# Performance work log

Measured on AMD Instinct MI355X. Metric: run time of the kernel, lower is better.

The kernel has to match this reference:

```python
import jax, jax.numpy as jnp
import numpy as np

B, S, H, E = 64, 512, 768, 8
HID = 256

def setup_inputs() -> dict:
    key = jax.random.key(0)
    ks = jax.random.split(key, 20)
    seq = jax.random.normal(ks[0], (B, S, H), dtype=jnp.float32)
    starts = jax.random.randint(ks[1], (B, E), 0, S - 16)
    spans = jax.random.randint(ks[2], (B, E), 0, 12)
    ends = jnp.minimum(starts + spans, S - 1)
    w = lambda k, shp: (jax.random.normal(k, shp, dtype=jnp.float32) * 0.02)
    return {
        "sequence_output": seq,
        "entity_start_positions": starts,
        "entity_end_positions": ends,
        "mW1": w(ks[3], (3 * H, HID)), "mb1": jnp.zeros((HID,), jnp.float32),
        "mW2": w(ks[4], (HID, 3)),     "mb2": jnp.zeros((3,), jnp.float32),
        "pW1": w(ks[5], (3 * H, HID)), "pb1": jnp.zeros((HID,), jnp.float32),
        "pW2": w(ks[6], (HID, 6)),     "pb2": jnp.zeros((6,), jnp.float32),
        "aW1": w(ks[7], (3 * H, HID)), "ab1": jnp.zeros((HID,), jnp.float32),
        "aW2": w(ks[8], (HID, 12)),    "ab2": jnp.zeros((12,), jnp.float32),
        "iW1": w(ks[9], (3 * H, HID)), "ib1": jnp.zeros((HID,), jnp.float32),
        "iW2": w(ks[10], (HID, 4)),    "ib2": jnp.zeros((4,), jnp.float32),
    }

def _mlp(x, W1, b1, W2, b2):
    return jax.nn.relu(x @ W1 + b1) @ W2 + b2  # dropout is inference no-op

def reference(sequence_output, entity_start_positions, entity_end_positions,
              mW1, mb1, mW2, mb2, pW1, pb1, pW2, pb2,
              aW1, ab1, aW2, ab2, iW1, ib1, iW2, ib2):
    Bs, Ss, Hs = sequence_output.shape
    dt = sequence_output.dtype
    # prefix sums: P[b, t] = sum of tokens [0, t)
    P = jnp.concatenate([jnp.zeros((Bs, 1, Hs), dt), jnp.cumsum(sequence_output, axis=1)], axis=1)  # [B,S+1,H]
    s = entity_start_positions  # [B,E]
    e = entity_end_positions    # [B,E]
    bidx = jnp.arange(Bs)[:, None]
    Ps = P[bidx, s]          # [B,E,H] sum of tokens [0, start)
    Pe1 = P[bidx, e + 1]     # [B,E,H] sum of tokens [0, end+1)
    Ptot = P[:, Ss][:, None, :]  # [B,1,H]
    left_n = s.astype(dt)[..., None]
    span_n = (e - s + 1).astype(dt)[..., None]
    right_cnt = (Ss - (e + 1))
    right_n = right_cnt.astype(dt)[..., None]
    left = jnp.where(s[..., None] > 0, Ps / jnp.maximum(left_n, 1.0), 0.0)
    span = (Pe1 - Ps) / span_n
    right = jnp.where(right_cnt[..., None] > 0, (Ptot - Pe1) / jnp.maximum(right_n, 1.0), 0.0)
    emb = jnp.concatenate([left, span, right], axis=-1).reshape(-1, 3 * Hs)  # [N, 3H]
    main_logits = _mlp(emb, mW1, mb1, mW2, mb2)            # [N,3]
    main_probs = jax.nn.softmax(main_logits, axis=-1)
    pred = jnp.argmax(main_probs, axis=-1)                 # [N]
    lp = jax.nn.sigmoid(_mlp(emb, pW1, pb1, pW2, pb2))     # [N,6]
    la = jax.nn.sigmoid(_mlp(emb, aW1, ab1, aW2, ab2))     # [N,12]
    li = jax.nn.sigmoid(_mlp(emb, iW1, ib1, iW2, ib2))     # [N,4]
    fp = jnp.pad(lp, ((0, 0), (0, 16)))
    fa = jnp.pad(la, ((0, 0), (6, 4)))
    fi = jnp.pad(li, ((0, 0), (18, 0)))
    r = pred[:, None]
    fine = jnp.where(r == 0, fp, jnp.where(r == 1, fa, fi))  # [N,22]
    return main_logits, main_probs, fine
```

## Files before the change

### kernel.cpp

```cpp
#include <hip/hip_runtime.h>

#define HH   768
#define SS   512
#define BB   64
#define NE   512
#define K3   2304
#define HID  256
#define NCH  16
#define CRW  32
#define NCOL 1280

typedef __attribute__((ext_vector_type(4))) float  f32x4;
typedef _Float16 f16;
typedef __attribute__((ext_vector_type(8))) _Float16 f16x8;
typedef __attribute__((ext_vector_type(4))) _Float16 f16x4;

__global__ __launch_bounds__(192) void k_scan(
    const float* __restrict__ seq, const int* __restrict__ starts,
    const int* __restrict__ ends, const float* __restrict__ pW1,
    const float* __restrict__ aW1, const float* __restrict__ iW1,
    const float* __restrict__ mW1,
    float* __restrict__ chunkSum, float* __restrict__ cap,
    f16* __restrict__ wT)
{
  __shared__ float Ls[48 * 65];
  const int bx = blockIdx.x;
  const int t  = threadIdx.x;

  if (bx < BB * NCH) {
    const int b = bx >> 4, c = bx & 15;
    int ev[16];
#pragma unroll
    for (int j = 0; j < 8; j++) {
      ev[j]     = starts[b * 8 + j];
      ev[8 + j] = ends[b * 8 + j] + 1;
    }
    unsigned rowhit = 0;
#pragma unroll
    for (int j = 0; j < 16; j++) {
      const int d = ev[j] - c * CRW;
      if ((unsigned)d < 32u) rowhit |= (1u << d);
    }
    const float* base = seq + ((size_t)(b * SS + c * CRW)) * HH + t * 4;
    f32x4 run = {0.f, 0.f, 0.f, 0.f};
#pragma unroll 8
    for (int r = 0; r < CRW; r++) {
      const int s = c * CRW + r;
      if (rowhit & (1u << r)) {
#pragma unroll
        for (int j = 0; j < 16; j++) {
          if (ev[j] == s)
            *(f32x4*)(cap + ((size_t)(b * 16 + j)) * HH + t * 4) = run;
        }
      }
      f32x4 v = *(const f32x4*)(base + (size_t)r * HH);
      run += v;
    }
    *(f32x4*)(chunkSum + ((size_t)(b * 16 + c)) * HH + t * 4) = run;
  } else {
    const int bi   = bx - BB * NCH;
    const int slot = bi / 192;
    const int r    = bi % 192;
    const int kt = r >> 2, nt = r & 3;
    const int k0 = kt * 48, n0 = nt * 64;
    const float* W = (slot == 0) ? pW1 : ((slot == 1) ? aW1 :
                     ((slot == 2) ? iW1 : mW1));
#pragma unroll
    for (int p = 0; p < 4; p++) {
      const int row = (t >> 4) + p * 12;
      const int col = (t & 15) * 4;
      f32x4 v = *(const f32x4*)(W + (size_t)(k0 + row) * HID + n0 + col);
      Ls[row * 65 + col + 0] = v.x;
      Ls[row * 65 + col + 1] = v.y;
      Ls[row * 65 + col + 2] = v.z;
      Ls[row * 65 + col + 3] = v.w;
    }
    __syncthreads();
    const int n = t / 3, u = t % 3;
#pragma unroll
    for (int j = 0; j < 2; j++) {
      const int kb = u * 16 + j * 8;
      f16x8 pk;
#pragma unroll
      for (int i = 0; i < 8; i++) {
        float x = Ls[(kb + i) * 65 + n];
        if (slot == 4) { const f16 h = (f16)x; x = x - (float)h; }
        pk[i] = (f16)x;
      }
      *(f16x8*)(wT + (size_t)(slot * 256 + n0 + n) * K3 + k0 + kb) = pk;
    }
  }
}

__global__ __launch_bounds__(192) void k_emb(
    const float* __restrict__ chunkSum, const float* __restrict__ cap,
    const int* __restrict__ starts, const int* __restrict__ ends,
    f16* __restrict__ embH)
{
  const int bx = blockIdx.x;
  const int t  = threadIdx.x;
  const int b = bx >> 3, e = bx & 7;
  const int s  = starts[b * 8 + e];
  const int en = ends[b * 8 + e];
  const int cs = s >> 5, ce = (en + 1) >> 5;

  const float* csb = chunkSum + (size_t)(b * 16) * HH + t * 4;
  f32x4 acc = {0.f, 0.f, 0.f, 0.f};
  f32x4 baseS = {0.f, 0.f, 0.f, 0.f}, baseE = {0.f, 0.f, 0.f, 0.f};
#pragma unroll
  for (int c = 0; c < 16; c++) {
    if (c == cs) baseS = acc;
    if (c == ce) baseE = acc;
    acc += *(const f32x4*)(csb + (size_t)c * HH);
  }
  f32x4 capS = *(const f32x4*)(cap + (size_t)(b * 16 + e) * HH + t * 4);
  f32x4 capE = *(const f32x4*)(cap + (size_t)(b * 16 + 8 + e) * HH + t * 4);
  f32x4 Ps = baseS + capS;
  f32x4 Pe = baseE + capE;
  f32x4 Pt = acc;

  f32x4 zero = {0.f, 0.f, 0.f, 0.f};
  f32x4 left = zero;
  if (s > 0) left = Ps * (1.0f / (float)s);
  f32x4 span = (Pe - Ps) * (1.0f / (float)(en - s + 1));
  const int rc = SS - (en + 1);
  f32x4 right = zero;
  if (rc > 0) right = (Pt - Pe) * (1.0f / (float)rc);

  f16* ob = embH + (size_t)bx * K3 + t * 4;
  f16x4 p0, p1, p2;
#pragma unroll
  for (int i = 0; i < 4; i++) {
    p0[i] = (f16)left[i];
    p1[i] = (f16)span[i];
    p2[i] = (f16)right[i];
  }
  *(f16x4*)(ob)        = p0;
  *(f16x4*)(ob + 768)  = p1;
  *(f16x4*)(ob + 1536) = p2;
}

__global__ __launch_bounds__(256) void k_gemm(
    const f16* __restrict__ embH, const f16* __restrict__ wT,
    float* __restrict__ Hall)
{
  __shared__ __align__(16) char smem[27648];
  const int bx0 = blockIdx.x;
  const int bx  = (bx0 & 7) * 40 + (bx0 >> 3);
  const int t  = threadIdx.x;
  const int mt = bx & 15, nt = bx >> 4;
  const int m0 = mt * 32, nG0 = nt * 64;

  const int l = t & 63, w = t >> 6;
  const int w2 = w & 1;
  const int kw = w >> 1;
  const int klane = l >> 4;
  const int lr = l & 15;
  f32x4 acc[2][2] = {};

  const int am = t >> 3, ako = (t & 7) * 8;
  const f16* gA = embH + (size_t)(m0 + am) * K3 + ako;
  const int aoff = am * 72 + ako;
  const int bn0 = t >> 3,        bko0 = (t & 7) * 8;
  const int bn1 = (t + 256) >> 3, bko1 = (t & 7) * 8;
  const f16* gB0 = wT + (size_t)(nG0 + bn0) * K3 + bko0;
  const f16* gB1 = wT + (size_t)(nG0 + bn1) * K3 + bko1;
  const int boff0 = bn0 * 72 + bko0, boff1 = bn1 * 72 + bko1;

  f16x8 pA, pB0, pB1, qA, qB0, qB1;

#define LOADSET(S, KT) { const int kn_ = (KT) * 64;                       \
    S##A  = *(const f16x8*)(gA  + kn_);                                   \
    S##B0 = *(const f16x8*)(gB0 + kn_);                                   \
    S##B1 = *(const f16x8*)(gB1 + kn_); }

#define WRITESET(S, BUF) { f16* An_ = (f16*)(smem + (BUF) * 13824);       \
    f16* Bn_ = An_ + 2304;                                                \
    *(f16x8*)(An_ + aoff)  = S##A;                                        \
    *(f16x8*)(Bn_ + boff0) = S##B0;                                       \
    *(f16x8*)(Bn_ + boff1) = S##B1; }

#define COMPUTE(BUF) { f16* Ac_ = (f16*)(smem + (BUF) * 13824);           \
    f16* Bc_ = Ac_ + 2304;                                                \
    const int koff_ = kw * 32 + klane * 8;                                \
    f16x8 aW[2], bE[2];                                                   \
    _Pragma("unroll")                                                     \
    for (int f = 0; f < 2; f++) {                                         \
      aW[f] = *(const f16x8*)(Bc_ + (w2 * 32 + f * 16 + lr) * 72 + koff_);\
      bE[f] = *(const f16x8*)(Ac_ + (f * 16 + lr) * 72 + koff_);          \
    }                                                                     \
    _Pragma("unroll")                                                     \
    for (int fn = 0; fn < 2; fn++)                                        \
      _Pragma("unroll")                                                   \
      for (int fm = 0; fm < 2; fm++)                                      \
        acc[fn][fm] = __builtin_amdgcn_mfma_f32_16x16x32_f16(             \
            aW[fn], bE[fm], acc[fn][fm], 0, 0, 0); }

  LOADSET(p, 0);
  LOADSET(q, 1);
  WRITESET(p, 0);
  __syncthreads();

  for (int kt = 0; kt < 36; kt += 2) {
    if (kt < 34) LOADSET(p, kt + 2);
    COMPUTE(0);
    WRITESET(q, 1);
    __syncthreads();
    if (kt < 34) LOADSET(q, kt + 3);
    COMPUTE(1);
    if (kt < 34) WRITESET(p, 0);
    __syncthreads();
  }
#undef LOADSET
#undef WRITESET
#undef COMPUTE

  float* Lt = (float*)smem;
  if (kw == 1) {
#pragma unroll
    for (int fn = 0; fn < 2; fn++)
#pragma unroll
      for (int fm = 0; fm < 2; fm++) {
        const int nl = w2 * 32 + fn * 16 + klane * 4;
        const int ml = fm * 16 + lr;
        *(f32x4*)(Lt + ml * 68 + nl) = acc[fn][fm];
      }
  }
  __syncthreads();
  if (kw == 0) {
#pragma unroll
    for (int fn = 0; fn < 2; fn++)
#pragma unroll
      for (int fm = 0; fm < 2; fm++) {
        const int nl = w2 * 32 + fn * 16 + klane * 4;
        const int ml = fm * 16 + lr;
        f32x4* pd = (f32x4*)(Lt + ml * 68 + nl);
        *pd = *pd + acc[fn][fm];
      }
  }
  __syncthreads();
  const int row = t >> 3, cb = (t & 7) * 8;
  float* dst = Hall + (size_t)(m0 + row) * NCOL + nG0 + cb;
  const float* src = Lt + row * 68 + cb;
  *(f32x4*)(dst)     = *(const f32x4*)(src);
  *(f32x4*)(dst + 4) = *(const f32x4*)(src + 4);
}

__global__ __launch_bounds__(256) void k_head(
    const float* __restrict__ Hall,
    const float* __restrict__ mb1, const float* __restrict__ mW2, const float* __restrict__ mb2,
    const float* __restrict__ pb1, const float* __restrict__ pW2, const float* __restrict__ pb2,
    const float* __restrict__ ab1, const float* __restrict__ aW2, const float* __restrict__ ab2,
    const float* __restrict__ ib1, const float* __restrict__ iW2, const float* __restrict__ ib2,
    float* __restrict__ out)
{
  __shared__ float red[4][15];
  const int m = blockIdx.x;
  const int t = threadIdx.x;
  const int l = t & 63, wi = t >> 6;
  const int n = t;
  const float* hrow = Hall + (size_t)m * NCOL;

  float h = hrow[768 + n] + hrow[1024 + n] + mb1[n];
  h = h > 0.f ? h : 0.f;
  float am0 = h * mW2[n * 3 + 0];
  float am1 = h * mW2[n * 3 + 1];
  float am2 = h * mW2[n * 3 + 2];

  float hp = hrow[n] + pb1[n];
  hp = hp > 0.f ? hp : 0.f;
  float ha = hrow[256 + n] + ab1[n];
  ha = ha > 0.f ? ha : 0.f;
  float hv = hrow[512 + n] + ib1[n];
  hv = hv > 0.f ? hv : 0.f;

#pragma unroll
  for (int d = 1; d < 64; d <<= 1) {
    am0 += __shfl_xor(am0, d);
    am1 += __shfl_xor(am1, d);
    am2 += __shfl_xor(am2, d);
  }
  if (l == 0) { red[wi][0] = am0; red[wi][1] = am1; red[wi][2] = am2; }
  __syncthreads();

  const float l0 = red[0][0] + red[1][0] + red[2][0] + red[3][0] + mb2[0];
  const float l1 = red[0][1] + red[1][1] + red[2][1] + red[3][1] + mb2[1];
  const float l2 = red[0][2] + red[1][2] + red[2][2] + red[3][2] + mb2[2];
  int pred = 0;
  {
    float pbv = l0;
    if (l1 > pbv) { pbv = l1; pred = 1; }
    if (l2 > pbv) { pbv = l2; pred = 2; }
  }

  if (pred == 0) {
    float ap[6];
#pragma unroll
    for (int o = 0; o < 6; o++) ap[o] = hp * pW2[n * 6 + o];
#pragma unroll
    for (int d = 1; d < 64; d <<= 1)
#pragma unroll
      for (int o = 0; o < 6; o++) ap[o] += __shfl_xor(ap[o], d);
    if (l == 0)
#pragma unroll
      for (int o = 0; o < 6; o++) red[wi][3 + o] = ap[o];
  } else if (pred == 1) {
    float aa[12];
#pragma unroll
    for (int o = 0; o < 12; o++) aa[o] = ha * aW2[n * 12 + o];
#pragma unroll
    for (int d = 1; d < 64; d <<= 1)
#pragma unroll
      for (int o = 0; o < 12; o++) aa[o] += __shfl_xor(aa[o], d);
    if (l == 0)
#pragma unroll
      for (int o = 0; o < 12; o++) red[wi][3 + o] = aa[o];
  } else {
    float ai[4];
#pragma unroll
    for (int o = 0; o < 4; o++) ai[o] = hv * iW2[n * 4 + o];
#pragma unroll
    for (int d = 1; d < 64; d <<= 1)
#pragma unroll
      for (int o = 0; o < 4; o++) ai[o] += __shfl_xor(ai[o], d);
    if (l == 0)
#pragma unroll
      for (int o = 0; o < 4; o++) red[wi][3 + o] = ai[o];
  }
  __syncthreads();

  if (t == 0) {
    const float mx = fmaxf(l0, fmaxf(l1, l2));
    const float e0 = expf(l0 - mx), e1 = expf(l1 - mx), e2 = expf(l2 - mx);
    const float inv = 1.0f / (e0 + e1 + e2);
    const float p0 = e0 * inv, p1 = e1 * inv, p2 = e2 * inv;

    out[m * 3 + 0] = l0;
    out[m * 3 + 1] = l1;
    out[m * 3 + 2] = l2;
    out[1536 + m * 3 + 0] = p0;
    out[1536 + m * 3 + 1] = p1;
    out[1536 + m * 3 + 2] = p2;

    float f[22];
#pragma unroll
    for (int j = 0; j < 22; j++) f[j] = 0.f;
    if (pred == 0) {
#pragma unroll
      for (int j = 0; j < 6; j++) {
        const float v = red[0][3 + j] + red[1][3 + j] + red[2][3 + j] + red[3][3 + j];
        f[j] = 1.0f / (1.0f + expf(-(v + pb2[j])));
      }
    } else if (pred == 1) {
#pragma unroll
      for (int j = 0; j < 12; j++) {
        const float v = red[0][3 + j] + red[1][3 + j] + red[2][3 + j] + red[3][3 + j];
        f[6 + j] = 1.0f / (1.0f + expf(-(v + ab2[j])));
      }
    } else {
#pragma unroll
      for (int j = 0; j < 4; j++) {
        const float v = red[0][3 + j] + red[1][3 + j] + red[2][3 + j] + red[3][3 + j];
        f[18 + j] = 1.0f / (1.0f + expf(-(v + ib2[j])));
      }
    }
#pragma unroll
    for (int j = 0; j < 22; j++) out[3072 + m * 22 + j] = f[j];
  }
}

extern "C" void kernel_launch(void* const* d_in, const int* in_sizes, int n_in,
                              void* d_out, int out_size, void* d_ws, size_t ws_size,
                              hipStream_t stream)
{
  const float* seq    = (const float*)d_in[0];
  const int*   starts = (const int*)d_in[1];
  const int*   ends   = (const int*)d_in[2];
  const float* mW1 = (const float*)d_in[3];
  const float* mb1 = (const float*)d_in[4];
  const float* mW2 = (const float*)d_in[5];
  const float* mb2 = (const float*)d_in[6];
  const float* pW1 = (const float*)d_in[7];
  const float* pb1 = (const float*)d_in[8];
  const float* pW2 = (const float*)d_in[9];
  const float* pb2 = (const float*)d_in[10];
  const float* aW1 = (const float*)d_in[11];
  const float* ab1 = (const float*)d_in[12];
  const float* aW2 = (const float*)d_in[13];
  const float* ab2 = (const float*)d_in[14];
  const float* iW1 = (const float*)d_in[15];
  const float* ib1 = (const float*)d_in[16];
  const float* iW2 = (const float*)d_in[17];
  const float* ib2 = (const float*)d_in[18];

  char* ws = (char*)d_ws;
  float* chunkSum = (float*)(ws);
  float* cap      = (float*)(ws + 3145728);
  f16*   embH     = (f16*)(ws + 6291456);
  f16*   wT       = (f16*)(ws + 8650752);
  float* Hall     = (float*)(ws + 14548992);

  k_scan<<<dim3(1984), dim3(192), 0, stream>>>(seq, starts, ends, pW1, aW1, iW1, mW1,
                                               chunkSum, cap, wT);
  k_emb<<<dim3(512), dim3(192), 0, stream>>>(chunkSum, cap, starts, ends, embH);
  k_gemm<<<dim3(320), dim3(256), 0, stream>>>(embH, wT, Hall);
  k_head<<<dim3(512), dim3(256), 0, stream>>>(Hall,
                                              mb1, mW2, mb2, pb1, pW2, pb2,
                                              ab1, aW2, ab2, ib1, iW2, ib2,
                                              (float*)d_out);
}
```

Before: 49.61 us.

## Split GEMM K dimension in two, merge emb blocks per batch, fuse hi/lo weight split

The GEMM now splits the K=2304 reduction into two halves across twice as many blocks (640). Each half writes its own partial Hall buffer, and the head kernel sums the two. The emb kernel goes from one block per entity to one block per batch: it stages the 16 chunk sums in shared memory and loops over 8 entities, so the chunk sums are read once per batch instead of once per entity. The scan kernel writes the fp16 high and low parts of mW1 from a single block, cutting the weight-transpose grid. The costs are extra Hall write traffic and a much smaller emb grid, only 64 blocks.

```diff
diff --git a/kernel.cpp b/kernel.cpp
--- a/kernel.cpp
+++ b/kernel.cpp
@@ -77,17 +77,30 @@
     }
     __syncthreads();
     const int n = t / 3, u = t % 3;
-#pragma unroll
-    for (int j = 0; j < 2; j++) {
-      const int kb = u * 16 + j * 8;
-      f16x8 pk;
-#pragma unroll
-      for (int i = 0; i < 8; i++) {
-        float x = Ls[(kb + i) * 65 + n];
-        if (slot == 4) { const f16 h = (f16)x; x = x - (float)h; }
-        pk[i] = (f16)x;
-      }
-      *(f16x8*)(wT + (size_t)(slot * 256 + n0 + n) * K3 + k0 + kb) = pk;
+    if (slot < 3) {
+#pragma unroll
+      for (int j = 0; j < 2; j++) {
+        const int kb = u * 16 + j * 8;
+        f16x8 pk;
+#pragma unroll
+        for (int i = 0; i < 8; i++) pk[i] = (f16)Ls[(kb + i) * 65 + n];
+        *(f16x8*)(wT + (size_t)(slot * 256 + n0 + n) * K3 + k0 + kb) = pk;
+      }
+    } else {
+#pragma unroll
+      for (int j = 0; j < 2; j++) {
+        const int kb = u * 16 + j * 8;
+        f16x8 ph, pl;
+#pragma unroll
+        for (int i = 0; i < 8; i++) {
+          const float x = Ls[(kb + i) * 65 + n];
+          const f16 h = (f16)x;
+          ph[i] = h;
+          pl[i] = (f16)(x - (float)h);
+        }
+        *(f16x8*)(wT + (size_t)(768  + n0 + n) * K3 + k0 + kb) = ph;
+        *(f16x8*)(wT + (size_t)(1024 + n0 + n) * K3 + k0 + kb) = pl;
+      }
     }
   }
 }
@@ -97,47 +110,55 @@
     const int* __restrict__ starts, const int* __restrict__ ends,
     f16* __restrict__ embH)
 {
-  const int bx = blockIdx.x;
-  const int t  = threadIdx.x;
-  const int b = bx >> 3, e = bx & 7;
-  const int s  = starts[b * 8 + e];
-  const int en = ends[b * 8 + e];
-  const int cs = s >> 5, ce = (en + 1) >> 5;
-
-  const float* csb = chunkSum + (size_t)(b * 16) * HH + t * 4;
-  f32x4 acc = {0.f, 0.f, 0.f, 0.f};
-  f32x4 baseS = {0.f, 0.f, 0.f, 0.f}, baseE = {0.f, 0.f, 0.f, 0.f};
-#pragma unroll
-  for (int c = 0; c < 16; c++) {
-    if (c == cs) baseS = acc;
-    if (c == ce) baseE = acc;
-    acc += *(const f32x4*)(csb + (size_t)c * HH);
-  }
-  f32x4 capS = *(const f32x4*)(cap + (size_t)(b * 16 + e) * HH + t * 4);
-  f32x4 capE = *(const f32x4*)(cap + (size_t)(b * 16 + 8 + e) * HH + t * 4);
-  f32x4 Ps = baseS + capS;
-  f32x4 Pe = baseE + capE;
-  f32x4 Pt = acc;
-
-  f32x4 zero = {0.f, 0.f, 0.f, 0.f};
-  f32x4 left = zero;
-  if (s > 0) left = Ps * (1.0f / (float)s);
-  f32x4 span = (Pe - Ps) * (1.0f / (float)(en - s + 1));
-  const int rc = SS - (en + 1);
-  f32x4 right = zero;
-  if (rc > 0) right = (Pt - Pe) * (1.0f / (float)rc);
-
-  f16* ob = embH + (size_t)bx * K3 + t * 4;
-  f16x4 p0, p1, p2;
-#pragma unroll
-  for (int i = 0; i < 4; i++) {
-    p0[i] = (f16)left[i];
-    p1[i] = (f16)span[i];
-    p2[i] = (f16)right[i];
-  }
-  *(f16x4*)(ob)        = p0;
-  *(f16x4*)(ob + 768)  = p1;
-  *(f16x4*)(ob + 1536) = p2;
+  __shared__ float Ls[16 * 768];
+  const int b = blockIdx.x;
+  const int t = threadIdx.x;
+
+#pragma unroll
+  for (int c = 0; c < 16; c++)
+    *(f32x4*)(Ls + c * 768 + t * 4) =
+        *(const f32x4*)(chunkSum + ((size_t)(b * 16 + c)) * HH + t * 4);
+  __syncthreads();
+
+  for (int e = 0; e < 8; e++) {
+    const int s  = starts[b * 8 + e];
+    const int en = ends[b * 8 + e];
+    const int cs = s >> 5, ce = (en + 1) >> 5;
+
+    f32x4 acc = {0.f, 0.f, 0.f, 0.f};
+    f32x4 baseS = {0.f, 0.f, 0.f, 0.f}, baseE = {0.f, 0.f, 0.f, 0.f};
+#pragma unroll
+    for (int c = 0; c < 16; c++) {
+      if (c == cs) baseS = acc;
+      if (c == ce) baseE = acc;
+      acc += *(const f32x4*)(Ls + c * 768 + t * 4);
+    }
+    f32x4 capS = *(const f32x4*)(cap + (size_t)(b * 16 + e) * HH + t * 4);
+    f32x4 capE = *(const f32x4*)(cap + (size_t)(b * 16 + 8 + e) * HH + t * 4);
+    f32x4 Ps = baseS + capS;
+    f32x4 Pe = baseE + capE;
+    f32x4 Pt = acc;
+
+    f32x4 zero = {0.f, 0.f, 0.f, 0.f};
+    f32x4 left = zero;
+    if (s > 0) left = Ps * (1.0f / (float)s);
+    f32x4 span = (Pe - Ps) * (1.0f / (float)(en - s + 1));
+    const int rc = SS - (en + 1);
+    f32x4 right = zero;
+    if (rc > 0) right = (Pt - Pe) * (1.0f / (float)rc);
+
+    f16* ob = embH + (size_t)(b * 8 + e) * K3 + t * 4;
+    f16x4 p0, p1, p2;
+#pragma unroll
+    for (int i = 0; i < 4; i++) {
+      p0[i] = (f16)left[i];
+      p1[i] = (f16)span[i];
+      p2[i] = (f16)right[i];
+    }
+    *(f16x4*)(ob)        = p0;
+    *(f16x4*)(ob + 768)  = p1;
+    *(f16x4*)(ob + 1536) = p2;
+  }
 }
 
 __global__ __launch_bounds__(256) void k_gemm(
@@ -146,10 +167,13 @@
 {
   __shared__ __align__(16) char smem[27648];
   const int bx0 = blockIdx.x;
-  const int bx  = (bx0 & 7) * 40 + (bx0 >> 3);
+  const int bx  = (bx0 & 7) * 80 + (bx0 >> 3);
   const int t  = threadIdx.x;
-  const int mt = bx & 15, nt = bx >> 4;
+  const int mt = bx & 15;
+  const int rest = bx >> 4;
+  const int ks = rest / 20, nt = rest % 20;
   const int m0 = mt * 32, nG0 = nt * 64;
+  const int kc0 = ks * 1152;
 
   const int l = t & 63, w = t >> 6;
   const int w2 = w & 1;
@@ -159,12 +183,12 @@
   f32x4 acc[2][2] = {};
 
   const int am = t >> 3, ako = (t & 7) * 8;
-  const f16* gA = embH + (size_t)(m0 + am) * K3 + ako;
+  const f16* gA = embH + (size_t)(m0 + am) * K3 + kc0 + ako;
   const int aoff = am * 72 + ako;
-  const int bn0 = t >> 3,        bko0 = (t & 7) * 8;
+  const int bn0 = t >> 3,         bko0 = (t & 7) * 8;
   const int bn1 = (t + 256) >> 3, bko1 = (t & 7) * 8;
-  const f16* gB0 = wT + (size_t)(nG0 + bn0) * K3 + bko0;
-  const f16* gB1 = wT + (size_t)(nG0 + bn1) * K3 + bko1;
+  const f16* gB0 = wT + (size_t)(nG0 + bn0) * K3 + kc0 + bko0;
+  const f16* gB1 = wT + (size_t)(nG0 + bn1) * K3 + kc0 + bko1;
   const int boff0 = bn0 * 72 + bko0, boff1 = bn1 * 72 + bko1;
 
   f16x8 pA, pB0, pB1, qA, qB0, qB1;
@@ -201,14 +225,14 @@
   WRITESET(p, 0);
   __syncthreads();
 
-  for (int kt = 0; kt < 36; kt += 2) {
-    if (kt < 34) LOADSET(p, kt + 2);
+  for (int kt = 0; kt < 18; kt += 2) {
+    if (kt < 16) LOADSET(p, kt + 2);
     COMPUTE(0);
     WRITESET(q, 1);
     __syncthreads();
-    if (kt < 34) LOADSET(q, kt + 3);
+    if (kt < 16) LOADSET(q, kt + 3);
     COMPUTE(1);
-    if (kt < 34) WRITESET(p, 0);
+    if (kt < 16) WRITESET(p, 0);
     __syncthreads();
   }
 #undef LOADSET
@@ -240,7 +264,7 @@
   }
   __syncthreads();
   const int row = t >> 3, cb = (t & 7) * 8;
-  float* dst = Hall + (size_t)(m0 + row) * NCOL + nG0 + cb;
+  float* dst = Hall + (size_t)ks * NE * NCOL + (size_t)(m0 + row) * NCOL + nG0 + cb;
   const float* src = Lt + row * 68 + cb;
   *(f32x4*)(dst)     = *(const f32x4*)(src);
   *(f32x4*)(dst + 4) = *(const f32x4*)(src + 4);
@@ -259,19 +283,20 @@
   const int t = threadIdx.x;
   const int l = t & 63, wi = t >> 6;
   const int n = t;
-  const float* hrow = Hall + (size_t)m * NCOL;
-
-  float h = hrow[768 + n] + hrow[1024 + n] + mb1[n];
+  const float* hrA = Hall + (size_t)m * NCOL;
+  const float* hrB = Hall + (size_t)NE * NCOL + (size_t)m * NCOL;
+
+  float h = (hrA[768 + n] + hrB[768 + n]) + (hrA[1024 + n] + hrB[1024 + n]) + mb1[n];
   h = h > 0.f ? h : 0.f;
   float am0 = h * mW2[n * 3 + 0];
   float am1 = h * mW2[n * 3 + 1];
   float am2 = h * mW2[n * 3 + 2];
 
-  float hp = hrow[n] + pb1[n];
+  float hp = (hrA[n] + hrB[n]) + pb1[n];
   hp = hp > 0.f ? hp : 0.f;
-  float ha = hrow[256 + n] + ab1[n];
+  float ha = (hrA[256 + n] + hrB[256 + n]) + ab1[n];
   ha = ha > 0.f ? ha : 0.f;
-  float hv = hrow[512 + n] + ib1[n];
+  float hv = (hrA[512 + n] + hrB[512 + n]) + ib1[n];
   hv = hv > 0.f ? hv : 0.f;
 
 #pragma unroll
@@ -400,10 +425,10 @@
   f16*   wT       = (f16*)(ws + 8650752);
   float* Hall     = (float*)(ws + 14548992);
 
-  k_scan<<<dim3(1984), dim3(192), 0, stream>>>(seq, starts, ends, pW1, aW1, iW1, mW1,
+  k_scan<<<dim3(1792), dim3(192), 0, stream>>>(seq, starts, ends, pW1, aW1, iW1, mW1,
                                                chunkSum, cap, wT);
-  k_emb<<<dim3(512), dim3(192), 0, stream>>>(chunkSum, cap, starts, ends, embH);
-  k_gemm<<<dim3(320), dim3(256), 0, stream>>>(embH, wT, Hall);
+  k_emb<<<dim3(64), dim3(192), 0, stream>>>(chunkSum, cap, starts, ends, embH);
+  k_gemm<<<dim3(640), dim3(256), 0, stream>>>(embH, wT, Hall);
   k_head<<<dim3(512), dim3(256), 0, stream>>>(Hall,
                                               mb1, mW2, mb2, pb1, pW2, pb2,
                                               ab1, aW2, ab2, ib1, iW2, ib2,
```

Measured after the change: 51.78 us. +4.4%, slower.
